# Optimization experiments

Measured on AMD Instinct MI355X. Metric: run time of the kernel, lower is better.

Reference implementation:

```python
import jax, jax.numpy as jnp
import numpy as np

N_HEAD = 16

def setup_inputs() -> dict:
    key = jax.random.key(0)
    k1, k2, k3 = jax.random.split(key, 3)
    B, S, D = 2, 2048, 1024
    std = 0.02
    return {
        "hidden_states": jax.random.normal(k1, (B, S, D), jnp.float32),
        "w_attn": jax.random.normal(k2, (D, 3 * D), jnp.float32) * std,
        "b_attn": jnp.zeros((3 * D,), jnp.float32),
        "w_proj": jax.random.normal(k3, (D, D), jnp.float32) * std,
        "b_proj": jnp.zeros((D,), jnp.float32),
    }

def reference(hidden_states, w_attn, b_attn, w_proj, b_proj):
    B, S, D = hidden_states.shape
    H = N_HEAD
    hd = D // H
    # fused qkv projection (Conv1D == x @ W + b)
    qkv = hidden_states @ w_attn + b_attn            # [B,S,3D]
    q, k, v = jnp.split(qkv, 3, axis=-1)
    def split_heads(t):
        return t.reshape(B, S, H, hd).transpose(0, 2, 1, 3)  # [B,H,S,hd]
    q, k, v = split_heads(q), split_heads(k), split_heads(v)
    # scores with scale = sqrt(head_dim)
    scores = jnp.einsum('bhqd,bhkd->bhqk', q, k) / jnp.sqrt(jnp.asarray(hd, q.dtype))
    causal = jnp.tril(jnp.ones((S, S), bool))
    mask_value = jnp.finfo(scores.dtype).min
    scores = jnp.where(causal, scores, mask_value)
    attn = jax.nn.softmax(scores, axis=-1)           # dropout p=0 (eval)
    out = jnp.einsum('bhqk,bhkd->bhqd', attn, v)     # [B,H,S,hd]
    out = out.transpose(0, 2, 1, 3).reshape(B, S, D)
    out = out @ w_proj + b_proj
    return out
```

## Files before the change

kernel.cpp:

```cpp
#include <hip/hip_runtime.h>

#define S_LEN 2048
#define D_MODEL 1024
#define NHEAD 16
#define HDIM 64
#define BATCH 2
#define M_ROWS (BATCH * S_LEN)
#define N_QKV (3 * D_MODEL)
#define QSCALE 0.18033688011112042f

typedef __attribute__((ext_vector_type(8))) short bf16x8;
typedef __attribute__((ext_vector_type(4))) short bf16x4;
typedef __attribute__((ext_vector_type(4))) float f32x4;

#if __has_builtin(__builtin_amdgcn_mfma_f32_16x16x16bf16_1k)
#define MFMA1616(A, B, C) __builtin_amdgcn_mfma_f32_16x16x16bf16_1k((A), (B), (C), 0, 0, 0)
#else
static __device__ __forceinline__ f32x4 mfma1616_asm(bf16x4 a, bf16x4 b, f32x4 c) {
  asm("v_mfma_f32_16x16x16_bf16 %0, %1, %2, %0" : "+v"(c) : "v"(a), "v"(b));
  return c;
}
#define MFMA1616(A, B, C) mfma1616_asm((A), (B), (C))
#endif

static __device__ __forceinline__ unsigned short f2bf(float f) {
  unsigned int u = __float_as_uint(f);
  u += 0x7FFFu + ((u >> 16) & 1u);
  return (unsigned short)(u >> 16);
}
static __device__ __forceinline__ unsigned int pkbf(float a, float b) {
  unsigned int ua = __float_as_uint(a) + 0x8000u;
  unsigned int ub = __float_as_uint(b) + 0x8000u;
  return __builtin_amdgcn_perm(ub, ua, 0x07060302u);
}

static __device__ __forceinline__ void async_cp16(unsigned short* lds, const unsigned short* g) {
  __builtin_amdgcn_global_load_lds((__attribute__((address_space(1))) void*)g,
                                   (__attribute__((address_space(3))) void*)lds, 16, 0, 0);
}

__global__ __launch_bounds__(256) void k_prep(const float* __restrict__ x,
                                              unsigned short* __restrict__ xb,
                                              const float* __restrict__ w_attn,
                                              unsigned short* __restrict__ wqkvT,
                                              const float* __restrict__ w_proj,
                                              unsigned short* __restrict__ wprojT) {
  __shared__ unsigned short T[32][33];
  const int blk = blockIdx.x;
  const int tid = threadIdx.x;
  if (blk < 4096) {
    int i = blk * 256 + tid;
    float4 v = ((const float4*)x)[i];
    ushort4 o;
    o.x = f2bf(v.x); o.y = f2bf(v.y); o.z = f2bf(v.z); o.w = f2bf(v.w);
    ((ushort4*)xb)[i] = o;
    return;
  }
  const float* w;
  unsigned short* wT;
  int bid, Ndim;
  if (blk < 7168) { bid = blk - 4096; w = w_attn; wT = wqkvT; Ndim = N_QKV; }
  else            { bid = blk - 7168; w = w_proj; wT = wprojT; Ndim = D_MODEL; }
  const int nb = Ndim / 32;
  const int n0 = (bid % nb) * 32, k0 = (bid / nb) * 32;
  const int tx = tid & 31, ty = tid >> 5;
#pragma unroll
  for (int j = 0; j < 4; ++j) {
    int r = ty + j * 8;
    T[r][tx] = f2bf(w[(size_t)(k0 + r) * Ndim + n0 + tx]);
  }
  __syncthreads();
#pragma unroll
  for (int j = 0; j < 4; ++j) {
    int r = ty + j * 8;
    wT[(size_t)(n0 + r) * D_MODEL + k0 + tx] = T[tx][r];
  }
}

__global__ __launch_bounds__(256) void k_gemm_qkv(const unsigned short* __restrict__ A,
                                                  const unsigned short* __restrict__ Bt,
                                                  const float* __restrict__ bias,
                                                  unsigned short* __restrict__ Qb,
                                                  unsigned short* __restrict__ Kbuf,
                                                  unsigned short* __restrict__ VTb) {
  __shared__ __align__(16) unsigned short As[2][128 * 32];
  __shared__ __align__(16) unsigned short Bs[2][128 * 32];
  const int tid = threadIdx.x;
  const int wid = tid >> 6, lane = tid & 63;
  const int lr = lane & 15, lg = lane >> 4;
  const int blk = blockIdx.x;
  const int xcd = blk & 7, idx = blk >> 3;
  const int bm = ((xcd & 3) * 8 + (idx & 7)) * 128;
  const int bn = ((xcd >> 2) * 12 + (idx >> 3)) * 128;
  const int wm = (wid >> 1) * 64, wn = (wid & 1) * 64;
  const int K = D_MODEL;
  const int c0 = tid, c1 = tid + 256;
  const size_t a0o = (size_t)(bm + (c0 >> 2)) * K + (c0 & 3) * 8;
  const size_t a1o = (size_t)(bm + (c1 >> 2)) * K + (c1 & 3) * 8;
  const size_t b0o = (size_t)(bn + (c0 >> 2)) * K + (c0 & 3) * 8;
  const size_t b1o = (size_t)(bn + (c1 >> 2)) * K + (c1 & 3) * 8;

  f32x4 acc[4][4] = {};

  async_cp16(&As[0][c0 * 8], &A[a0o]);
  async_cp16(&As[0][c1 * 8], &A[a1o]);
  async_cp16(&Bs[0][c0 * 8], &Bt[b0o]);
  async_cp16(&Bs[0][c1 * 8], &Bt[b1o]);

  for (int k0 = 0; k0 < K; k0 += 32) {
    const int p = (k0 >> 5) & 1;
    __syncthreads();
    if (k0 + 32 < K) {
      async_cp16(&As[p ^ 1][c0 * 8], &A[a0o + k0 + 32]);
      async_cp16(&As[p ^ 1][c1 * 8], &A[a1o + k0 + 32]);
      async_cp16(&Bs[p ^ 1][c0 * 8], &Bt[b0o + k0 + 32]);
      async_cp16(&Bs[p ^ 1][c1 * 8], &Bt[b1o + k0 + 32]);
    }
    bf16x8 af[4], bfr[4];
#pragma unroll
    for (int i = 0; i < 4; ++i) af[i] = *(const bf16x8*)&As[p][(wm + i * 16 + lr) * 32 + lg * 8];
#pragma unroll
    for (int t = 0; t < 4; ++t) bfr[t] = *(const bf16x8*)&Bs[p][(wn + t * 16 + lr) * 32 + lg * 8];
#pragma unroll
    for (int i = 0; i < 4; ++i)
#pragma unroll
      for (int t = 0; t < 4; ++t)
        acc[i][t] = __builtin_amdgcn_mfma_f32_16x16x32_bf16(af[i], bfr[t], acc[i][t], 0, 0, 0);
  }
#pragma unroll
  for (int i = 0; i < 4; ++i) {
#pragma unroll
    for (int t = 0; t < 4; ++t) {
      int n = bn + wn + t * 16 + lr;
      int part = n >> 10, rem = n & 1023;
      int h = rem >> 6, d = rem & 63;
      float bv = bias[n];
      int row0 = bm + wm + i * 16 + lg * 4;
      int bb = row0 >> 11, s0 = row0 & 2047;
      if (part == 2) {
        ushort4 vv;
        vv.x = f2bf(acc[i][t][0] + bv);
        vv.y = f2bf(acc[i][t][1] + bv);
        vv.z = f2bf(acc[i][t][2] + bv);
        vv.w = f2bf(acc[i][t][3] + bv);
        int s0x = s0 ^ ((d & 8) ? 4 : 0);
        *(ushort4*)&VTb[(((size_t)(bb << 4) + h) * HDIM + d) * S_LEN + s0x] = vv;
      } else {
        unsigned short* dst = (part == 0) ? Qb : Kbuf;
        float sc = (part == 0) ? QSCALE : 1.0f;
#pragma unroll
        for (int r = 0; r < 4; ++r)
          dst[(((size_t)(bb << 4) + h) * S_LEN + (s0 + r)) * HDIM + d] = f2bf((acc[i][t][r] + bv) * sc);
      }
    }
  }
}

__global__ __launch_bounds__(256) void k_gemm_proj(const unsigned short* __restrict__ A,
                                                   const unsigned short* __restrict__ Bt,
                                                   const float* __restrict__ bias,
                                                   float* __restrict__ out) {
  __shared__ __align__(16) unsigned short As[2][128 * 32];
  __shared__ __align__(16) unsigned short Bs[2][128 * 32];
  const int tid = threadIdx.x;
  const int wid = tid >> 6, lane = tid & 63;
  const int lr = lane & 15, lg = lane >> 4;
  const int blk = blockIdx.x;
  const int xcd = blk & 7, idx = blk >> 3;
  const int bm = (xcd * 4 + (idx & 3)) * 128;
  const int bn = (idx >> 2) * 128;
  const int wm = (wid >> 1) * 64, wn = (wid & 1) * 64;
  const int K = D_MODEL;
  const int c0 = tid, c1 = tid + 256;
  const size_t a0o = (size_t)(bm + (c0 >> 2)) * K + (c0 & 3) * 8;
  const size_t a1o = (size_t)(bm + (c1 >> 2)) * K + (c1 & 3) * 8;
  const size_t b0o = (size_t)(bn + (c0 >> 2)) * K + (c0 & 3) * 8;
  const size_t b1o = (size_t)(bn + (c1 >> 2)) * K + (c1 & 3) * 8;

  f32x4 acc[4][4] = {};

  async_cp16(&As[0][c0 * 8], &A[a0o]);
  async_cp16(&As[0][c1 * 8], &A[a1o]);
  async_cp16(&Bs[0][c0 * 8], &Bt[b0o]);
  async_cp16(&Bs[0][c1 * 8], &Bt[b1o]);

  for (int k0 = 0; k0 < K; k0 += 32) {
    const int p = (k0 >> 5) & 1;
    __syncthreads();
    if (k0 + 32 < K) {
      async_cp16(&As[p ^ 1][c0 * 8], &A[a0o + k0 + 32]);
      async_cp16(&As[p ^ 1][c1 * 8], &A[a1o + k0 + 32]);
      async_cp16(&Bs[p ^ 1][c0 * 8], &Bt[b0o + k0 + 32]);
      async_cp16(&Bs[p ^ 1][c1 * 8], &Bt[b1o + k0 + 32]);
    }
    bf16x8 af[4], bfr[4];
#pragma unroll
    for (int i = 0; i < 4; ++i) af[i] = *(const bf16x8*)&As[p][(wm + i * 16 + lr) * 32 + lg * 8];
#pragma unroll
    for (int t = 0; t < 4; ++t) bfr[t] = *(const bf16x8*)&Bs[p][(wn + t * 16 + lr) * 32 + lg * 8];
#pragma unroll
    for (int i = 0; i < 4; ++i)
#pragma unroll
      for (int t = 0; t < 4; ++t)
        acc[i][t] = __builtin_amdgcn_mfma_f32_16x16x32_bf16(af[i], bfr[t], acc[i][t], 0, 0, 0);
  }
#pragma unroll
  for (int i = 0; i < 4; ++i) {
#pragma unroll
    for (int t = 0; t < 4; ++t) {
      int n = bn + wn + t * 16 + lr;
      float bv = bias[n];
#pragma unroll
      for (int r = 0; r < 4; ++r) {
        int row = bm + wm + i * 16 + lg * 4 + r;
        out[(size_t)row * D_MODEL + n] = acc[i][t][r] + bv;
      }
    }
  }
}

__global__ __launch_bounds__(256, 5) void k_attn10(const unsigned short* __restrict__ Qb,
                                                   const unsigned short* __restrict__ Kb,
                                                   const unsigned short* __restrict__ VT,
                                                   unsigned short* __restrict__ AO,
                                                   float* __restrict__ Pp) {
  const int tid = threadIdx.x;
  const int wid = tid >> 6, lane = tid & 63;
  const int lr = lane & 15, quad = lane >> 4;
  const int blk = blockIdx.x;
  const int bh = blk & 31;
  const int id = blk >> 5;
  const int b = bh >> 4, h = bh & 15;

  int t, c;
  if (id < 17)       { t = 31 - id; c = 0; }
  else if (id == 17) { t = 31;      c = 1; }
  else {
    const int k = id - 18, p_ = k >> 1;
    if (k & 1) { t = 30 - p_; c = 1; }
    else       { t = 14 - p_; c = 0; }
  }
  const int sL = t * 4 + wid;
  const int R = sL * 16;
  const int kt0 = c << 4;
  const int ktend = (c == 0) ? ((t + 1 < 16) ? (t + 1) : 16) : (t + 1);

  __shared__ __align__(16) unsigned short Ks[2][64 * 64];
  __shared__ __align__(16) unsigned short Vs[2][64 * 64];

  const unsigned short* Kbh = Kb + (size_t)bh * S_LEN * HDIM;
  const unsigned short* VTbh = VT + (size_t)bh * HDIM * S_LEN;

  bf16x8 qf[2];
#pragma unroll
  for (int dh = 0; dh < 2; ++dh)
    qf[dh] = *(const bf16x8*)&Qb[((size_t)bh * S_LEN + R + lr) * HDIM + dh * 32 + quad * 8];

  f32x4 Ot[4] = {};
  float ls = 0.f;

  const int srow = lane >> 3;
  const int scol = ((lane & 7) ^ srow) * 8;

  {
    const int kg0 = kt0 * 64;
#pragma unroll
    for (int j = 0; j < 2; ++j) {
      const int r0 = wid * 16 + j * 8;
      async_cp16(&Ks[0][r0 * 64 + lane * 8], &Kbh[(size_t)(kg0 + r0 + srow) * HDIM + scol]);
      async_cp16(&Vs[0][r0 * 64 + lane * 8], &VTbh[(size_t)(r0 + srow) * S_LEN + kg0 + scol]);
    }
  }

  for (int kt = kt0; kt < ktend; ++kt) {
    const int k0 = kt * 64;
    const int p = kt & 1;
    __syncthreads();
    if (kt + 1 < ktend) {
      const int kn = k0 + 64;
#pragma unroll
      for (int j = 0; j < 2; ++j) {
        const int r0 = wid * 16 + j * 8;
        async_cp16(&Ks[p ^ 1][r0 * 64 + lane * 8], &Kbh[(size_t)(kn + r0 + srow) * HDIM + scol]);
        async_cp16(&Vs[p ^ 1][r0 * 64 + lane * 8], &VTbh[(size_t)(r0 + srow) * S_LEN + kn + scol]);
      }
    }

    bf16x8 kf[4][2];
#pragma unroll
    for (int kg = 0; kg < 4; ++kg)
#pragma unroll
      for (int dh = 0; dh < 2; ++dh)
        kf[kg][dh] = *(const bf16x8*)&Ks[p][(kg * 16 + lr) * 64 + (((dh * 4 + quad) ^ (lr & 7)) * 8)];

    f32x4 Sv[4];
#pragma unroll
    for (int kg = 0; kg < 4; ++kg) {
      f32x4 a = {};
      a = __builtin_amdgcn_mfma_f32_16x16x32_bf16(kf[kg][0], qf[0], a, 0, 0, 0);
      a = __builtin_amdgcn_mfma_f32_16x16x32_bf16(kf[kg][1], qf[1], a, 0, 0, 0);
      Sv[kg] = a;
    }
    if (k0 + 63 > R) {
      const int q = R + lr;
#pragma unroll
      for (int kg = 0; kg < 4; ++kg)
#pragma unroll
        for (int r = 0; r < 4; ++r)
          if (k0 + kg * 16 + quad * 4 + r > q) Sv[kg][r] = -1e30f;
    }
    bf16x4 pf[4];
#pragma unroll
    for (int kg = 0; kg < 4; ++kg) {
      float e0 = __builtin_amdgcn_exp2f(Sv[kg][0]);
      float e1 = __builtin_amdgcn_exp2f(Sv[kg][1]);
      float e2 = __builtin_amdgcn_exp2f(Sv[kg][2]);
      float e3 = __builtin_amdgcn_exp2f(Sv[kg][3]);
      ls += (e0 + e1) + (e2 + e3);
      union { bf16x4 v; unsigned int u[2]; } pu;
      pu.u[0] = pkbf(e0, e1);
      pu.u[1] = pkbf(e2, e3);
      pf[kg] = pu.v;
    }

#pragma unroll
    for (int dg = 0; dg < 4; ++dg) {
      bf16x4 vf[4];
#pragma unroll
      for (int kg = 0; kg < 4; ++kg)
        vf[kg] = *(const bf16x4*)&Vs[p][(dg * 16 + lr) * 64 +
                                        (((kg * 2 + (quad >> 1)) ^ (lr & 7)) * 8) +
                                        (((quad & 1) ^ ((lr >> 3) & 1)) * 4)];
#pragma unroll
      for (int kg = 0; kg < 4; ++kg)
        Ot[dg] = MFMA1616(vf[kg], pf[kg], Ot[dg]);
    }
  }

  ls += __shfl_xor(ls, 16);
  ls += __shfl_xor(ls, 32);

  if (t < 16) {
    const float rl = __builtin_amdgcn_rcpf(ls);
    const int s = R + lr;
#pragma unroll
    for (int dg = 0; dg < 4; ++dg) {
      const size_t o = ((size_t)b * S_LEN + s) * D_MODEL + h * 64 + dg * 16 + quad * 4;
      *(unsigned int*)&AO[o]     = pkbf(Ot[dg][0] * rl, Ot[dg][1] * rl);
      *(unsigned int*)&AO[o + 2] = pkbf(Ot[dg][2] * rl, Ot[dg][3] * rl);
    }
  } else {
    float* P = Pp + ((size_t)((bh * 64 + (sL - 64)) * 2 + c)) * (16 * 68) + lr * 68;
#pragma unroll
    for (int dg = 0; dg < 4; ++dg)
      *(f32x4*)&P[dg * 16 + quad * 4] = Ot[dg];
    if (quad == 0) { P[64] = 0.f; P[65] = ls; }
  }
}

__global__ __launch_bounds__(256) void k_combine(const float* __restrict__ Pp,
                                                 unsigned short* __restrict__ AO) {
  const int lane = threadIdx.x & 63;
  const int sid = blockIdx.x * 4 + (threadIdx.x >> 6);
  const int bh = sid >> 6, jrel = sid & 63;
  const int b = bh >> 4, h = bh & 15;
  const int r = lane & 15, cg = lane >> 4;
  const float* P0 = Pp + ((size_t)(bh * 64 + jrel) * 2) * (16 * 68) + r * 68;
  const float* P1 = P0 + 16 * 68;
  const float m0 = P0[64], l0 = P0[65];
  const float m1 = P1[64], l1 = P1[65];
  const float M = fmaxf(m0, m1);
  const float w0 = __builtin_amdgcn_exp2f(m0 - M);
  const float w1 = __builtin_amdgcn_exp2f(m1 - M);
  const float rl = __builtin_amdgcn_rcpf(l0 * w0 + l1 * w1);
  const int s = (64 + jrel) * 16 + r;
  const size_t o0 = ((size_t)b * S_LEN + s) * D_MODEL + h * 64 + cg * 16;
#pragma unroll
  for (int q4 = 0; q4 < 4; ++q4) {
    f32x4 a = *(const f32x4*)&P0[cg * 16 + q4 * 4];
    f32x4 b4 = *(const f32x4*)&P1[cg * 16 + q4 * 4];
    float o0v = (a[0] * w0 + b4[0] * w1) * rl;
    float o1v = (a[1] * w0 + b4[1] * w1) * rl;
    float o2v = (a[2] * w0 + b4[2] * w1) * rl;
    float o3v = (a[3] * w0 + b4[3] * w1) * rl;
    *(unsigned int*)&AO[o0 + q4 * 4]     = pkbf(o0v, o1v);
    *(unsigned int*)&AO[o0 + q4 * 4 + 2] = pkbf(o2v, o3v);
  }
}

extern "C" void kernel_launch(void* const* d_in, const int* in_sizes, int n_in,
                              void* d_out, int out_size, void* d_ws, size_t ws_size,
                              hipStream_t stream) {
  const float* x      = (const float*)d_in[0];
  const float* w_attn = (const float*)d_in[1];
  const float* b_attn = (const float*)d_in[2];
  const float* w_proj = (const float*)d_in[3];
  const float* b_proj = (const float*)d_in[4];
  float* out = (float*)d_out;

  unsigned short* ws     = (unsigned short*)d_ws;
  unsigned short* xb     = ws;
  unsigned short* wqkvT  = xb + (size_t)M_ROWS * D_MODEL;
  unsigned short* wprojT = wqkvT + (size_t)N_QKV * D_MODEL;
  unsigned short* Qb     = wprojT + (size_t)D_MODEL * D_MODEL;
  unsigned short* Kb     = Qb + (size_t)M_ROWS * D_MODEL;
  unsigned short* VT     = Kb + (size_t)M_ROWS * D_MODEL;
  float* Pp              = (float*)(VT + (size_t)M_ROWS * D_MODEL);
  unsigned short* AO     = xb;

  k_prep<<<8192, 256, 0, stream>>>(x, xb, w_attn, wqkvT, w_proj, wprojT);
  k_gemm_qkv<<<768, 256, 0, stream>>>(xb, wqkvT, b_attn, Qb, Kb, VT);
  k_attn10<<<1536, 256, 0, stream>>>(Qb, Kb, VT, AO, Pp);
  k_combine<<<512, 256, 0, stream>>>(Pp, AO);
  k_gemm_proj<<<256, 256, 0, stream>>>(AO, wprojT, b_proj, out);
}
```

Measured before the change: 174.0 us.

## Split attention KV range into chunks of eight tiles with multi-way combine

Attention work per query tile is split into up to four KV chunks of eight tiles instead of two halves of sixteen, with a new block schedule and a combine kernel that sums up to four partials. This aims to balance load across the causal triangle and raise parallelism. It also precomputes LDS offsets, bumps wave priority around MFMA sections, and uses the hardware bf16 pack instruction. The cost is more partial-result traffic and a larger combine pass.

Result: slower. 180.5 us (+3.7%).

```diff
diff --git a/kernel.cpp b/kernel.cpp
--- a/kernel.cpp
+++ b/kernel.cpp
@@ -32,6 +32,11 @@
   unsigned int ua = __float_as_uint(a) + 0x8000u;
   unsigned int ub = __float_as_uint(b) + 0x8000u;
   return __builtin_amdgcn_perm(ub, ua, 0x07060302u);
+}
+static __device__ __forceinline__ unsigned int cvtpk(float a, float b) {
+  unsigned int r;
+  asm("v_cvt_pk_bf16_f32 %0, %1, %2" : "=v"(r) : "v"(a), "v"(b));
+  return r;
 }
 
 static __device__ __forceinline__ void async_cp16(unsigned short* lds, const unsigned short* g) {
@@ -219,7 +224,7 @@
   }
 }
 
-__global__ __launch_bounds__(256, 5) void k_attn10(const unsigned short* __restrict__ Qb,
+__global__ __launch_bounds__(256, 5) void k_attn11(const unsigned short* __restrict__ Qb,
                                                    const unsigned short* __restrict__ Kb,
                                                    const unsigned short* __restrict__ VT,
                                                    unsigned short* __restrict__ AO,
@@ -233,17 +238,17 @@
   const int b = bh >> 4, h = bh & 15;
 
   int t, c;
-  if (id < 17)       { t = 31 - id; c = 0; }
-  else if (id == 17) { t = 31;      c = 1; }
-  else {
-    const int k = id - 18, p_ = k >> 1;
-    if (k & 1) { t = 30 - p_; c = 1; }
-    else       { t = 14 - p_; c = 0; }
-  }
+  if (id < 25)       { c = 0; t = 7 + id; }
+  else if (id < 42)  { c = 1; t = 15 + (id - 25); }
+  else if (id < 51)  { c = 2; t = 23 + (id - 42); }
+  else if (id == 51) { c = 3; t = 31; }
+  else { const int j = id - 52; c = j / 7; t = 8 * c + 6 - (j % 7); }
+
   const int sL = t * 4 + wid;
   const int R = sL * 16;
-  const int kt0 = c << 4;
-  const int ktend = (c == 0) ? ((t + 1 < 16) ? (t + 1) : 16) : (t + 1);
+  const int kt0 = c << 3;
+  const int tend = t + 1;
+  const int ktend = (kt0 + 8 < tend) ? (kt0 + 8) : tend;
 
   __shared__ __align__(16) unsigned short Ks[2][64 * 64];
   __shared__ __align__(16) unsigned short Vs[2][64 * 64];
@@ -256,44 +261,65 @@
   for (int dh = 0; dh < 2; ++dh)
     qf[dh] = *(const bf16x8*)&Qb[((size_t)bh * S_LEN + R + lr) * HDIM + dh * 32 + quad * 8];
 
+  const int qh = quad >> 1;
+  const int hs = (quad & 1) ^ ((lr >> 3) & 1);
+  int koff[8], voff[16];
+#pragma unroll
+  for (int kg = 0; kg < 4; ++kg)
+#pragma unroll
+    for (int dh = 0; dh < 2; ++dh)
+      koff[kg * 2 + dh] = (kg * 16 + lr) * 64 + (((dh * 4 + quad) ^ (lr & 7)) * 8);
+#pragma unroll
+  for (int dg = 0; dg < 4; ++dg)
+#pragma unroll
+    for (int kg = 0; kg < 4; ++kg)
+      voff[dg * 4 + kg] = (dg * 16 + lr) * 64 + (((kg * 2 + qh) ^ (lr & 7)) * 8) + hs * 4;
+
   f32x4 Ot[4] = {};
   float ls = 0.f;
 
   const int srow = lane >> 3;
   const int scol = ((lane & 7) ^ srow) * 8;
-
-  {
-    const int kg0 = kt0 * 64;
-#pragma unroll
-    for (int j = 0; j < 2; ++j) {
-      const int r0 = wid * 16 + j * 8;
-      async_cp16(&Ks[0][r0 * 64 + lane * 8], &Kbh[(size_t)(kg0 + r0 + srow) * HDIM + scol]);
-      async_cp16(&Vs[0][r0 * 64 + lane * 8], &VTbh[(size_t)(r0 + srow) * S_LEN + kg0 + scol]);
-    }
-  }
+  const int ldst0 = (wid * 16) * 64 + lane * 8;
+  const int ldst1 = (wid * 16 + 8) * 64 + lane * 8;
+
+  const unsigned short* kst0 = Kbh + ((size_t)(kt0 * 64 + wid * 16 + srow)) * HDIM + scol;
+  const unsigned short* kst1 = kst0 + 8 * HDIM;
+  const unsigned short* vst0 = VTbh + (size_t)(wid * 16 + srow) * S_LEN + kt0 * 64 + scol;
+  const unsigned short* vst1 = vst0 + 8 * S_LEN;
+
+  async_cp16(&Ks[0][ldst0], kst0);
+  async_cp16(&Ks[0][ldst1], kst1);
+  async_cp16(&Vs[0][ldst0], vst0);
+  async_cp16(&Vs[0][ldst1], vst1);
 
   for (int kt = kt0; kt < ktend; ++kt) {
     const int k0 = kt * 64;
     const int p = kt & 1;
     __syncthreads();
     if (kt + 1 < ktend) {
-      const int kn = k0 + 64;
-#pragma unroll
-      for (int j = 0; j < 2; ++j) {
-        const int r0 = wid * 16 + j * 8;
-        async_cp16(&Ks[p ^ 1][r0 * 64 + lane * 8], &Kbh[(size_t)(kn + r0 + srow) * HDIM + scol]);
-        async_cp16(&Vs[p ^ 1][r0 * 64 + lane * 8], &VTbh[(size_t)(r0 + srow) * S_LEN + kn + scol]);
-      }
-    }
+      kst0 += 64 * HDIM; kst1 += 64 * HDIM;
+      vst0 += 64;        vst1 += 64;
+      unsigned short* Kn = &Ks[p ^ 1][0];
+      unsigned short* Vn = &Vs[p ^ 1][0];
+      async_cp16(&Kn[ldst0], kst0);
+      async_cp16(&Kn[ldst1], kst1);
+      async_cp16(&Vn[ldst0], vst0);
+      async_cp16(&Vn[ldst1], vst1);
+    }
+
+    const unsigned short* Ksp = &Ks[p][0];
+    const unsigned short* Vsp = &Vs[p][0];
 
     bf16x8 kf[4][2];
 #pragma unroll
     for (int kg = 0; kg < 4; ++kg)
 #pragma unroll
       for (int dh = 0; dh < 2; ++dh)
-        kf[kg][dh] = *(const bf16x8*)&Ks[p][(kg * 16 + lr) * 64 + (((dh * 4 + quad) ^ (lr & 7)) * 8)];
+        kf[kg][dh] = *(const bf16x8*)&Ksp[koff[kg * 2 + dh]];
 
     f32x4 Sv[4];
+    __builtin_amdgcn_s_setprio(1);
 #pragma unroll
     for (int kg = 0; kg < 4; ++kg) {
       f32x4 a = {};
@@ -301,6 +327,7 @@
       a = __builtin_amdgcn_mfma_f32_16x16x32_bf16(kf[kg][1], qf[1], a, 0, 0, 0);
       Sv[kg] = a;
     }
+    __builtin_amdgcn_s_setprio(0);
     if (k0 + 63 > R) {
       const int q = R + lr;
 #pragma unroll
@@ -318,43 +345,43 @@
       float e3 = __builtin_amdgcn_exp2f(Sv[kg][3]);
       ls += (e0 + e1) + (e2 + e3);
       union { bf16x4 v; unsigned int u[2]; } pu;
-      pu.u[0] = pkbf(e0, e1);
-      pu.u[1] = pkbf(e2, e3);
+      pu.u[0] = cvtpk(e0, e1);
+      pu.u[1] = cvtpk(e2, e3);
       pf[kg] = pu.v;
     }
 
+    __builtin_amdgcn_s_setprio(1);
 #pragma unroll
     for (int dg = 0; dg < 4; ++dg) {
       bf16x4 vf[4];
 #pragma unroll
       for (int kg = 0; kg < 4; ++kg)
-        vf[kg] = *(const bf16x4*)&Vs[p][(dg * 16 + lr) * 64 +
-                                        (((kg * 2 + (quad >> 1)) ^ (lr & 7)) * 8) +
-                                        (((quad & 1) ^ ((lr >> 3) & 1)) * 4)];
+        vf[kg] = *(const bf16x4*)&Vsp[voff[dg * 4 + kg]];
 #pragma unroll
       for (int kg = 0; kg < 4; ++kg)
         Ot[dg] = MFMA1616(vf[kg], pf[kg], Ot[dg]);
     }
+    __builtin_amdgcn_s_setprio(0);
   }
 
   ls += __shfl_xor(ls, 16);
   ls += __shfl_xor(ls, 32);
 
-  if (t < 16) {
+  if (t < 8) {
     const float rl = __builtin_amdgcn_rcpf(ls);
     const int s = R + lr;
 #pragma unroll
     for (int dg = 0; dg < 4; ++dg) {
       const size_t o = ((size_t)b * S_LEN + s) * D_MODEL + h * 64 + dg * 16 + quad * 4;
-      *(unsigned int*)&AO[o]     = pkbf(Ot[dg][0] * rl, Ot[dg][1] * rl);
-      *(unsigned int*)&AO[o + 2] = pkbf(Ot[dg][2] * rl, Ot[dg][3] * rl);
+      *(unsigned int*)&AO[o]     = cvtpk(Ot[dg][0] * rl, Ot[dg][1] * rl);
+      *(unsigned int*)&AO[o + 2] = cvtpk(Ot[dg][2] * rl, Ot[dg][3] * rl);
     }
   } else {
-    float* P = Pp + ((size_t)((bh * 64 + (sL - 64)) * 2 + c)) * (16 * 68) + lr * 68;
+    float* P = Pp + ((size_t)((bh * 96 + (sL - 32)) * 4 + c)) * (16 * 68) + lr * 68;
 #pragma unroll
     for (int dg = 0; dg < 4; ++dg)
       *(f32x4*)&P[dg * 16 + quad * 4] = Ot[dg];
-    if (quad == 0) { P[64] = 0.f; P[65] = ls; }
+    if (quad == 0) P[64] = ls;
   }
 }
 
@@ -362,30 +389,31 @@
                                                  unsigned short* __restrict__ AO) {
   const int lane = threadIdx.x & 63;
   const int sid = blockIdx.x * 4 + (threadIdx.x >> 6);
-  const int bh = sid >> 6, jrel = sid & 63;
+  const int bh = sid / 96, ps = sid - bh * 96;
   const int b = bh >> 4, h = bh & 15;
   const int r = lane & 15, cg = lane >> 4;
-  const float* P0 = Pp + ((size_t)(bh * 64 + jrel) * 2) * (16 * 68) + r * 68;
-  const float* P1 = P0 + 16 * 68;
-  const float m0 = P0[64], l0 = P0[65];
-  const float m1 = P1[64], l1 = P1[65];
-  const float M = fmaxf(m0, m1);
-  const float w0 = __builtin_amdgcn_exp2f(m0 - M);
-  const float w1 = __builtin_amdgcn_exp2f(m1 - M);
-  const float rl = __builtin_amdgcn_rcpf(l0 * w0 + l1 * w1);
-  const int s = (64 + jrel) * 16 + r;
-  const size_t o0 = ((size_t)b * S_LEN + s) * D_MODEL + h * 64 + cg * 16;
-#pragma unroll
-  for (int q4 = 0; q4 < 4; ++q4) {
-    f32x4 a = *(const f32x4*)&P0[cg * 16 + q4 * 4];
-    f32x4 b4 = *(const f32x4*)&P1[cg * 16 + q4 * 4];
-    float o0v = (a[0] * w0 + b4[0] * w1) * rl;
-    float o1v = (a[1] * w0 + b4[1] * w1) * rl;
-    float o2v = (a[2] * w0 + b4[2] * w1) * rl;
-    float o3v = (a[3] * w0 + b4[3] * w1) * rl;
-    *(unsigned int*)&AO[o0 + q4 * 4]     = pkbf(o0v, o1v);
-    *(unsigned int*)&AO[o0 + q4 * 4 + 2] = pkbf(o2v, o3v);
-  }
+  const int nc = ((ps >> 2) + 16) >> 3;
+  const float* P = Pp + (size_t)(sid * 4) * (16 * 68) + r * 68;
+  f32x4 a0 = {}, a1 = {}, a2 = {}, a3 = {};
+  float l = 0.f;
+  for (int c = 0; c < nc; ++c, P += 16 * 68) {
+    a0 += *(const f32x4*)&P[cg * 16 + 0];
+    a1 += *(const f32x4*)&P[cg * 16 + 4];
+    a2 += *(const f32x4*)&P[cg * 16 + 8];
+    a3 += *(const f32x4*)&P[cg * 16 + 12];
+    l += P[64];
+  }
+  const float rl = __builtin_amdgcn_rcpf(l);
+  const int s = (ps + 32) * 16 + r;
+  const size_t o = ((size_t)b * S_LEN + s) * D_MODEL + h * 64 + cg * 16;
+  *(unsigned int*)&AO[o]      = cvtpk(a0[0] * rl, a0[1] * rl);
+  *(unsigned int*)&AO[o + 2]  = cvtpk(a0[2] * rl, a0[3] * rl);
+  *(unsigned int*)&AO[o + 4]  = cvtpk(a1[0] * rl, a1[1] * rl);
+  *(unsigned int*)&AO[o + 6]  = cvtpk(a1[2] * rl, a1[3] * rl);
+  *(unsigned int*)&AO[o + 8]  = cvtpk(a2[0] * rl, a2[1] * rl);
+  *(unsigned int*)&AO[o + 10] = cvtpk(a2[2] * rl, a2[3] * rl);
+  *(unsigned int*)&AO[o + 12] = cvtpk(a3[0] * rl, a3[1] * rl);
+  *(unsigned int*)&AO[o + 14] = cvtpk(a3[2] * rl, a3[3] * rl);
 }
 
 extern "C" void kernel_launch(void* const* d_in, const int* in_sizes, int n_in,
@@ -410,7 +438,7 @@
 
   k_prep<<<8192, 256, 0, stream>>>(x, xb, w_attn, wqkvT, w_proj, wprojT);
   k_gemm_qkv<<<768, 256, 0, stream>>>(xb, wqkvT, b_attn, Qb, Kb, VT);
-  k_attn10<<<1536, 256, 0, stream>>>(Qb, Kb, VT, AO, Pp);
-  k_combine<<<512, 256, 0, stream>>>(Pp, AO);
+  k_attn11<<<2560, 256, 0, stream>>>(Qb, Kb, VT, AO, Pp);
+  k_combine<<<768, 256, 0, stream>>>(Pp, AO);
   k_gemm_proj<<<256, 256, 0, stream>>>(AO, wprojT, b_proj, out);
 }
```

## Process two query subtiles per wave to reuse K/V tiles across 128-row blocks

Applied to the files above, without the earlier changes.

The attention kernel now gives each wave two 16-row query subtiles (128 query rows per block instead of 64), so each K/V tile loaded into LDS feeds twice the MFMA work. The grid halves and the work-scheduling map is recomputed for the larger tiles, with per-subtile causal skipping. It also swaps the manual bf16 packing for the hardware v_cvt_pk_bf16_f32 instruction and adds s_setprio around the MFMA sections. Register pressure rises (occupancy hint drops from 5 to 3), and fewer, larger blocks may balance less evenly.

Result: no change. 172.8 us (-0.7%).

```diff
diff --git a/kernel.cpp b/kernel.cpp
--- a/kernel.cpp
+++ b/kernel.cpp
@@ -32,6 +32,11 @@
   unsigned int ua = __float_as_uint(a) + 0x8000u;
   unsigned int ub = __float_as_uint(b) + 0x8000u;
   return __builtin_amdgcn_perm(ub, ua, 0x07060302u);
+}
+static __device__ __forceinline__ unsigned int cvtpk(float a, float b) {
+  unsigned int r;
+  asm("v_cvt_pk_bf16_f32 %0, %1, %2" : "=v"(r) : "v"(a), "v"(b));
+  return r;
 }
 
 static __device__ __forceinline__ void async_cp16(unsigned short* lds, const unsigned short* g) {
@@ -219,7 +224,7 @@
   }
 }
 
-__global__ __launch_bounds__(256, 5) void k_attn10(const unsigned short* __restrict__ Qb,
+__global__ __launch_bounds__(256, 3) void k_attn14(const unsigned short* __restrict__ Qb,
                                                    const unsigned short* __restrict__ Kb,
                                                    const unsigned short* __restrict__ VT,
                                                    unsigned short* __restrict__ AO,
@@ -232,18 +237,17 @@
   const int id = blk >> 5;
   const int b = bh >> 4, h = bh & 15;
 
-  int t, c;
-  if (id < 17)       { t = 31 - id; c = 0; }
-  else if (id == 17) { t = 31;      c = 1; }
+  int T, c;
+  if (id < 9)       { T = 7 + id; c = 0; }
+  else if (id == 9) { T = 15;     c = 1; }
   else {
-    const int k = id - 18, p_ = k >> 1;
-    if (k & 1) { t = 30 - p_; c = 1; }
-    else       { t = 14 - p_; c = 0; }
-  }
-  const int sL = t * 4 + wid;
-  const int R = sL * 16;
+    const int j = id - 10, p_ = j >> 1;
+    if (j & 1) { T = 14 - p_; c = 1; }
+    else       { T = 6 - p_;  c = 0; }
+  }
   const int kt0 = c << 4;
-  const int ktend = (c == 0) ? ((t + 1 < 16) ? (t + 1) : 16) : (t + 1);
+  const int tiles = 2 * T + 2;
+  const int ktend = (c == 0) ? (tiles < 16 ? tiles : 16) : tiles;
 
   __shared__ __align__(16) unsigned short Ks[2][64 * 64];
   __shared__ __align__(16) unsigned short Vs[2][64 * 64];
@@ -251,13 +255,17 @@
   const unsigned short* Kbh = Kb + (size_t)bh * S_LEN * HDIM;
   const unsigned short* VTbh = VT + (size_t)bh * HDIM * S_LEN;
 
-  bf16x8 qf[2];
-#pragma unroll
-  for (int dh = 0; dh < 2; ++dh)
-    qf[dh] = *(const bf16x8*)&Qb[((size_t)bh * S_LEN + R + lr) * HDIM + dh * 32 + quad * 8];
-
-  f32x4 Ot[4] = {};
-  float ls = 0.f;
+  const int R0 = T * 128 + wid * 32;
+
+  bf16x8 qf[2][2];
+#pragma unroll
+  for (int st = 0; st < 2; ++st)
+#pragma unroll
+    for (int dh = 0; dh < 2; ++dh)
+      qf[st][dh] = *(const bf16x8*)&Qb[((size_t)bh * S_LEN + R0 + st * 16 + lr) * HDIM + dh * 32 + quad * 8];
+
+  f32x4 Ot[2][4] = {};
+  float ls[2] = {0.f, 0.f};
 
   const int srow = lane >> 3;
   const int scol = ((lane & 7) ^ srow) * 8;
@@ -285,6 +293,7 @@
         async_cp16(&Vs[p ^ 1][r0 * 64 + lane * 8], &VTbh[(size_t)(r0 + srow) * S_LEN + kn + scol]);
       }
     }
+    if (k0 > R0 + 31) continue;
 
     bf16x8 kf[4][2];
 #pragma unroll
@@ -293,36 +302,48 @@
       for (int dh = 0; dh < 2; ++dh)
         kf[kg][dh] = *(const bf16x8*)&Ks[p][(kg * 16 + lr) * 64 + (((dh * 4 + quad) ^ (lr & 7)) * 8)];
 
-    f32x4 Sv[4];
-#pragma unroll
-    for (int kg = 0; kg < 4; ++kg) {
-      f32x4 a = {};
-      a = __builtin_amdgcn_mfma_f32_16x16x32_bf16(kf[kg][0], qf[0], a, 0, 0, 0);
-      a = __builtin_amdgcn_mfma_f32_16x16x32_bf16(kf[kg][1], qf[1], a, 0, 0, 0);
-      Sv[kg] = a;
-    }
-    if (k0 + 63 > R) {
-      const int q = R + lr;
-#pragma unroll
-      for (int kg = 0; kg < 4; ++kg)
-#pragma unroll
-        for (int r = 0; r < 4; ++r)
-          if (k0 + kg * 16 + quad * 4 + r > q) Sv[kg][r] = -1e30f;
-    }
-    bf16x4 pf[4];
-#pragma unroll
-    for (int kg = 0; kg < 4; ++kg) {
-      float e0 = __builtin_amdgcn_exp2f(Sv[kg][0]);
-      float e1 = __builtin_amdgcn_exp2f(Sv[kg][1]);
-      float e2 = __builtin_amdgcn_exp2f(Sv[kg][2]);
-      float e3 = __builtin_amdgcn_exp2f(Sv[kg][3]);
-      ls += (e0 + e1) + (e2 + e3);
-      union { bf16x4 v; unsigned int u[2]; } pu;
-      pu.u[0] = pkbf(e0, e1);
-      pu.u[1] = pkbf(e2, e3);
-      pf[kg] = pu.v;
-    }
-
+    bf16x4 pf[2][4];
+    bool act[2];
+#pragma unroll
+    for (int st = 0; st < 2; ++st) {
+      const int R = R0 + st * 16;
+      act[st] = (k0 <= R + 15);
+      if (!act[st]) continue;
+      f32x4 Sv[4];
+      __builtin_amdgcn_s_setprio(1);
+#pragma unroll
+      for (int kg = 0; kg < 4; ++kg) {
+        f32x4 a = {};
+        a = __builtin_amdgcn_mfma_f32_16x16x32_bf16(kf[kg][0], qf[st][0], a, 0, 0, 0);
+        a = __builtin_amdgcn_mfma_f32_16x16x32_bf16(kf[kg][1], qf[st][1], a, 0, 0, 0);
+        Sv[kg] = a;
+      }
+      __builtin_amdgcn_s_setprio(0);
+      if (k0 + 63 > R) {
+        const int q = R + lr;
+#pragma unroll
+        for (int kg = 0; kg < 4; ++kg)
+#pragma unroll
+          for (int r = 0; r < 4; ++r)
+            if (k0 + kg * 16 + quad * 4 + r > q) Sv[kg][r] = -1e30f;
+      }
+      float rs = ls[st];
+#pragma unroll
+      for (int kg = 0; kg < 4; ++kg) {
+        float e0 = __builtin_amdgcn_exp2f(Sv[kg][0]);
+        float e1 = __builtin_amdgcn_exp2f(Sv[kg][1]);
+        float e2 = __builtin_amdgcn_exp2f(Sv[kg][2]);
+        float e3 = __builtin_amdgcn_exp2f(Sv[kg][3]);
+        rs += (e0 + e1) + (e2 + e3);
+        union { bf16x4 v; unsigned int u[2]; } pu;
+        pu.u[0] = cvtpk(e0, e1);
+        pu.u[1] = cvtpk(e2, e3);
+        pf[st][kg] = pu.v;
+      }
+      ls[st] = rs;
+    }
+
+    __builtin_amdgcn_s_setprio(1);
 #pragma unroll
     for (int dg = 0; dg < 4; ++dg) {
       bf16x4 vf[4];
@@ -332,29 +353,44 @@
                                         (((kg * 2 + (quad >> 1)) ^ (lr & 7)) * 8) +
                                         (((quad & 1) ^ ((lr >> 3) & 1)) * 4)];
 #pragma unroll
-      for (int kg = 0; kg < 4; ++kg)
-        Ot[dg] = MFMA1616(vf[kg], pf[kg], Ot[dg]);
-    }
-  }
-
-  ls += __shfl_xor(ls, 16);
-  ls += __shfl_xor(ls, 32);
-
-  if (t < 16) {
-    const float rl = __builtin_amdgcn_rcpf(ls);
-    const int s = R + lr;
-#pragma unroll
-    for (int dg = 0; dg < 4; ++dg) {
-      const size_t o = ((size_t)b * S_LEN + s) * D_MODEL + h * 64 + dg * 16 + quad * 4;
-      *(unsigned int*)&AO[o]     = pkbf(Ot[dg][0] * rl, Ot[dg][1] * rl);
-      *(unsigned int*)&AO[o + 2] = pkbf(Ot[dg][2] * rl, Ot[dg][3] * rl);
+      for (int st = 0; st < 2; ++st) {
+        if (!act[st]) continue;
+#pragma unroll
+        for (int kg = 0; kg < 4; ++kg)
+          Ot[st][dg] = MFMA1616(vf[kg], pf[st][kg], Ot[st][dg]);
+      }
+    }
+    __builtin_amdgcn_s_setprio(0);
+  }
+
+#pragma unroll
+  for (int st = 0; st < 2; ++st) {
+    ls[st] += __shfl_xor(ls[st], 16);
+    ls[st] += __shfl_xor(ls[st], 32);
+  }
+
+  if (T < 8) {
+#pragma unroll
+    for (int st = 0; st < 2; ++st) {
+      const float rl = __builtin_amdgcn_rcpf(ls[st]);
+      const int s = R0 + st * 16 + lr;
+#pragma unroll
+      for (int dg = 0; dg < 4; ++dg) {
+        const size_t o = ((size_t)b * S_LEN + s) * D_MODEL + h * 64 + dg * 16 + quad * 4;
+        *(unsigned int*)&AO[o]     = cvtpk(Ot[st][dg][0] * rl, Ot[st][dg][1] * rl);
+        *(unsigned int*)&AO[o + 2] = cvtpk(Ot[st][dg][2] * rl, Ot[st][dg][3] * rl);
+      }
     }
   } else {
-    float* P = Pp + ((size_t)((bh * 64 + (sL - 64)) * 2 + c)) * (16 * 68) + lr * 68;
-#pragma unroll
-    for (int dg = 0; dg < 4; ++dg)
-      *(f32x4*)&P[dg * 16 + quad * 4] = Ot[dg];
-    if (quad == 0) { P[64] = 0.f; P[65] = ls; }
+#pragma unroll
+    for (int st = 0; st < 2; ++st) {
+      const int sL = T * 8 + wid * 2 + st;
+      float* P = Pp + ((size_t)((bh * 64 + (sL - 64)) * 2 + c)) * (16 * 68) + lr * 68;
+#pragma unroll
+      for (int dg = 0; dg < 4; ++dg)
+        *(f32x4*)&P[dg * 16 + quad * 4] = Ot[st][dg];
+      if (quad == 0) { P[64] = 0.f; P[65] = ls[st]; }
+    }
   }
 }
 
@@ -410,7 +446,7 @@
 
   k_prep<<<8192, 256, 0, stream>>>(x, xb, w_attn, wqkvT, w_proj, wprojT);
   k_gemm_qkv<<<768, 256, 0, stream>>>(xb, wqkvT, b_attn, Qb, Kb, VT);
-  k_attn10<<<1536, 256, 0, stream>>>(Qb, Kb, VT, AO, Pp);
+  k_attn14<<<768, 256, 0, stream>>>(Qb, Kb, VT, AO, Pp);
   k_combine<<<512, 256, 0, stream>>>(Pp, AO);
   k_gemm_proj<<<256, 256, 0, stream>>>(AO, wprojT, b_proj, out);
 }
```
